# Optimization experiments

Hardware: AMD Instinct MI355X
Metric: run time of the kernel (lower is better)

Reference implementation:

```python
import jax, jax.numpy as jnp
import numpy as np

B, T, C, H = 4, 2048, 1024, 16
HD = C // H  # head_size = 64
EPS = 1e-5


def setup_inputs() -> dict:
    key = jax.random.key(0)
    ks = jax.random.split(key, 16)
    s_c = 1.0 / np.sqrt(C)
    s_4c = 1.0 / np.sqrt(4 * C)
    return {
        "x": jax.random.normal(ks[0], (B, T, C), jnp.float32),
        # per-head projections, stored [H, C, HD] (already in x@W orientation)
        "wq": jax.random.uniform(ks[1], (H, C, HD), jnp.float32, -s_c, s_c),
        "wk": jax.random.uniform(ks[2], (H, C, HD), jnp.float32, -s_c, s_c),
        "wv": jax.random.uniform(ks[3], (H, C, HD), jnp.float32, -s_c, s_c),
        "w_proj": jax.random.uniform(ks[4], (C, C), jnp.float32, -s_c, s_c),
        "b_proj": jax.random.uniform(ks[5], (C,), jnp.float32, -s_c, s_c),
        "w1": jax.random.uniform(ks[6], (C, 4 * C), jnp.float32, -s_c, s_c),
        "b1": jax.random.uniform(ks[7], (4 * C,), jnp.float32, -s_c, s_c),
        "w2": jax.random.uniform(ks[8], (4 * C, C), jnp.float32, -s_4c, s_4c),
        "b2": jax.random.uniform(ks[9], (C,), jnp.float32, -s_4c, s_4c),
        "ln1_g": jnp.ones((C,), jnp.float32),
        "ln1_b": jnp.zeros((C,), jnp.float32),
        "ln2_g": jnp.ones((C,), jnp.float32),
        "ln2_b": jnp.zeros((C,), jnp.float32),
    }


def layer_norm(x, g, b):
    mu = jnp.mean(x, axis=-1, keepdims=True)
    var = jnp.mean(jnp.square(x - mu), axis=-1, keepdims=True)
    return (x - mu) * jax.lax.rsqrt(var + EPS) * g + b


def reference(x, wq, wk, wv, w_proj, b_proj, w1, b1, w2, b2, ln1_g, ln1_b, ln2_g, ln2_b):
    Bc, Tc, Cc = x.shape
    h = layer_norm(x, ln1_g, ln1_b)
    q = jnp.einsum("btc,hcd->bhtd", h, wq)
    k = jnp.einsum("btc,hcd->bhtd", h, wk)
    v = jnp.einsum("btc,hcd->bhtd", h, wv)
    scale = HD ** -0.5
    wei = jnp.einsum("bhtd,bhsd->bhts", q, k) * scale  # [B,H,T,T]
    causal = jnp.tril(jnp.ones((Tc, Tc), bool))
    wei = jnp.where(causal, wei, -jnp.inf)
    wei = jax.nn.softmax(wei, axis=-1)
    att = jnp.einsum("bhts,bhsd->bhtd", wei, v)
    att = att.transpose(0, 2, 1, 3).reshape(Bc, Tc, Cc)  # concat heads
    x = x + att @ w_proj + b_proj
    h2 = layer_norm(x, ln2_g, ln2_b)
    ff = jax.nn.relu(h2 @ w1 + b1) @ w2 + b2
    return x + ff
```

## Files before the change

### kernel.cpp

```cpp
#include <hip/hip_runtime.h>


#define B_ 4
#define T_ 2048
#define C_ 1024
#define H_ 16
#define BT_ 8192

typedef __attribute__((ext_vector_type(8))) __bf16 bf16x8;
typedef __attribute__((ext_vector_type(4))) __bf16 bf16x4;
typedef __attribute__((ext_vector_type(4))) float f32x4;

#define WAIT_LGKM0 asm volatile("s_waitcnt lgkmcnt(0)" ::: "memory")
#define WAIT_VM4 asm volatile("s_waitcnt vmcnt(4)" ::: "memory")
#define WAIT_VM0 asm volatile("s_waitcnt vmcnt(0)" ::: "memory")

__device__ __forceinline__ void gload_lds16(const void* g, void* l) {
  __builtin_amdgcn_global_load_lds((const __attribute__((address_space(1))) void*)g,
                                   (__attribute__((address_space(3))) void*)l, 16, 0, 0);
}

__device__ __forceinline__ void block_sync() {
  asm volatile("" ::: "memory");
  __builtin_amdgcn_s_barrier();
  asm volatile("" ::: "memory");
}

__global__ __launch_bounds__(256) void transpose_f32_bf16(
    const float* __restrict__ in, __bf16* __restrict__ out,
    int R, int Cc, long inBatch, long outBatch) {
  __shared__ float tile[32][33];
  const int tx = threadIdx.x, ty = threadIdx.y;
  in += (long)blockIdx.z * inBatch;
  out += (long)blockIdx.z * outBatch;
  const int r0 = blockIdx.y * 32, c0 = blockIdx.x * 32;
#pragma unroll
  for (int i = 0; i < 4; i++)
    tile[ty + i * 8][tx] = in[(long)(r0 + ty + i * 8) * Cc + c0 + tx];
  __syncthreads();
#pragma unroll
  for (int i = 0; i < 4; i++)
    out[(long)(c0 + ty + i * 8) * R + r0 + tx] = (__bf16)tile[tx][ty + i * 8];
}

__global__ __launch_bounds__(256) void ln_fwd(const float* __restrict__ x,
                                              const float* __restrict__ g,
                                              const float* __restrict__ bta,
                                              __bf16* __restrict__ out) {
  const long row = blockIdx.x;
  const int tid = threadIdx.x;
  float4 v = ((const float4*)(x + row * C_))[tid];
  float vals[4] = {v.x, v.y, v.z, v.w};
  float s = vals[0] + vals[1] + vals[2] + vals[3];
  float s2 = vals[0] * vals[0] + vals[1] * vals[1] + vals[2] * vals[2] + vals[3] * vals[3];
#pragma unroll
  for (int o = 1; o < 64; o <<= 1) {
    s += __shfl_xor(s, o);
    s2 += __shfl_xor(s2, o);
  }
  __shared__ float red[8];
  const int lane = tid & 63, wid = tid >> 6;
  if (lane == 0) { red[wid] = s; red[wid + 4] = s2; }
  __syncthreads();
  const float S = red[0] + red[1] + red[2] + red[3];
  const float S2 = red[4] + red[5] + red[6] + red[7];
  const float mu = S * (1.0f / C_);
  const float var = S2 * (1.0f / C_) - mu * mu;
  const float rs = rsqrtf(var + 1e-5f);
  bf16x4 o4;
#pragma unroll
  for (int j = 0; j < 4; j++) {
    const int c = tid * 4 + j;
    o4[j] = (__bf16)((vals[j] - mu) * rs * g[c] + bta[c]);
  }
  *(bf16x4*)(out + row * C_ + tid * 4) = o4;
}

template <int OUT_BF16, int RELU, int HAS_BIAS, int HAS_RES, int TRANSO>
__global__ __launch_bounds__(256, 2) void gemm_bt(
    const __bf16* __restrict__ A, const __bf16* __restrict__ Bt, void* outp,
    const float* __restrict__ bias, const float* resid, int M, int N, int K) {
  __shared__ __bf16 As[128 * 32];
  __shared__ __bf16 Bs[128 * 32];
  const int tid = threadIdx.x, lane = tid & 63, wid = tid >> 6;
  const long mBase = (long)blockIdx.y * 128, nBase = (long)blockIdx.x * 128;
  const int wm = wid >> 1, wn = wid & 1;
  const int l15 = lane & 15, kHalf = (lane >> 4) * 8;
  f32x4 acc[4][4] = {};
  const int sRow = wid * 16 + (lane >> 2);
  const int sCol = (lane & 3) * 8;
  const __bf16* aP = A + (mBase + sRow) * (long)K + sCol;
  const __bf16* bP = Bt + (nBase + sRow) * (long)K + sCol;
  const int ldsOff = sRow * 32 + sCol;
  for (int kt = 0; kt < K; kt += 32) {
    gload_lds16(aP, As + ldsOff);
    gload_lds16(aP + 64 * (long)K, As + ldsOff + 2048);
    gload_lds16(bP, Bs + ldsOff);
    gload_lds16(bP + 64 * (long)K, Bs + ldsOff + 2048);
    aP += 32; bP += 32;
    __syncthreads();
    bf16x8 af[4], bfr[4];
#pragma unroll
    for (int mi = 0; mi < 4; mi++)
      af[mi] = *(const bf16x8*)&As[(wm * 64 + mi * 16 + l15) * 32 + kHalf];
#pragma unroll
    for (int ni = 0; ni < 4; ni++)
      bfr[ni] = *(const bf16x8*)&Bs[(wn * 64 + ni * 16 + l15) * 32 + kHalf];
#pragma unroll
    for (int mi = 0; mi < 4; mi++)
#pragma unroll
      for (int ni = 0; ni < 4; ni++)
        acc[mi][ni] = __builtin_amdgcn_mfma_f32_16x16x32_bf16(af[mi], bfr[ni], acc[mi][ni], 0, 0, 0);
    __syncthreads();
  }
#pragma unroll
  for (int mi = 0; mi < 4; mi++) {
#pragma unroll
    for (int ni = 0; ni < 4; ni++) {
      const long row0 = mBase + wm * 64 + mi * 16 + (lane >> 4) * 4;
      const long col = nBase + wn * 64 + ni * 16 + l15;
#pragma unroll
      for (int r = 0; r < 4; r++) {
        float vv = acc[mi][ni][r];
        if (HAS_BIAS) vv += bias[col];
        if (HAS_RES) vv += resid[(row0 + r) * N + col];
        if (RELU) vv = fmaxf(vv, 0.0f);
        if (OUT_BF16) {
          if (TRANSO) ((__bf16*)outp)[col * (long)M + row0 + r] = (__bf16)vv;
          else ((__bf16*)outp)[(row0 + r) * N + col] = (__bf16)vv;
        } else {
          ((float*)outp)[(row0 + r) * N + col] = vv;
        }
      }
    }
  }
}

template <int EPI>
__global__ __launch_bounds__(512, 2) void gemm256(
    const __bf16* __restrict__ A, const __bf16* __restrict__ Bt,
    void* out0, void* out1, void* out2,
    const float* __restrict__ bias, int M, int N, int K) {
  __shared__ __bf16 sm[3 * 16384];
  const int tid = threadIdx.x, lane = tid & 63, wid = tid >> 6;
  const int wm = wid >> 2, wn = wid & 3;
  const int l15 = lane & 15, qtr = lane >> 4;
  const long mBase = (long)blockIdx.y * 256, nBase = (long)blockIdx.x * 256;
  const int NT = K >> 5;

  f32x4 acc[8][4] = {};

  const int posOff = (qtr ^ ((l15 >> 1) & 3)) * 8;
  const int aBase = (wm * 128 + l15) * 32 + posOff;
  const int bBase = (wn * 64 + l15) * 32 + posOff;

  const int trow = tid >> 2;
  const long coff = (long)(((tid & 3) ^ ((tid >> 3) & 3)) * 8);
  const __bf16* aS0 = A + (mBase + trow) * (long)K + coff;
  const __bf16* aS1 = aS0 + 128 * (long)K;
  const __bf16* bS0 = Bt + (nBase + trow) * (long)K + coff;
  const __bf16* bS1 = bS0 + 128 * (long)K;

  {
    __bf16* d0 = &sm[0];
    gload_lds16(aS0, d0 + tid * 8);
    gload_lds16(aS1, d0 + 4096 + tid * 8);
    gload_lds16(bS0, d0 + 8192 + tid * 8);
    gload_lds16(bS1, d0 + 12288 + tid * 8);
    __bf16* d1 = &sm[16384];
    gload_lds16(aS0 + 32, d1 + tid * 8);
    gload_lds16(aS1 + 32, d1 + 4096 + tid * 8);
    gload_lds16(bS0 + 32, d1 + 8192 + tid * 8);
    gload_lds16(bS1 + 32, d1 + 12288 + tid * 8);
  }
  WAIT_VM4;
  block_sync();

  int sl = 0;
  for (int t = 0; t < NT; ++t) {
    const __bf16* sA = &sm[sl * 16384];
    const __bf16* sB = sA + 8192;
    const int slN = (sl + 2 >= 3) ? sl - 1 : sl + 2;
    __bf16* stA = &sm[slN * 16384];
    __bf16* stB = stA + 8192;
    const long kc = (long)(t + 2) * 32;
    const bool doStage = (t + 2 < NT);

    bf16x8 bfr[4], af[4];
#pragma unroll
    for (int cf = 0; cf < 4; cf++) bfr[cf] = *(const bf16x8*)&sB[bBase + cf * 512];
#pragma unroll
    for (int rf = 0; rf < 4; rf++) af[rf] = *(const bf16x8*)&sA[aBase + rf * 512];
    if (doStage) {
      gload_lds16(aS0 + kc, stA + tid * 8);
      gload_lds16(aS1 + kc, stA + 4096 + tid * 8);
    }
    block_sync();
    WAIT_LGKM0;
    __builtin_amdgcn_s_setprio(1);
#pragma unroll
    for (int rf = 0; rf < 4; rf++)
#pragma unroll
      for (int cf = 0; cf < 4; cf++)
        acc[rf][cf] = __builtin_amdgcn_mfma_f32_16x16x32_bf16(af[rf], bfr[cf], acc[rf][cf], 0, 0, 0);
    __builtin_amdgcn_s_setprio(0);
    block_sync();

#pragma unroll
    for (int rf = 0; rf < 4; rf++) af[rf] = *(const bf16x8*)&sA[aBase + 2048 + rf * 512];
    if (doStage) {
      gload_lds16(bS0 + kc, stB + tid * 8);
      gload_lds16(bS1 + kc, stB + 4096 + tid * 8);
      WAIT_VM4;
    } else {
      WAIT_VM0;
    }
    block_sync();
    WAIT_LGKM0;
    __builtin_amdgcn_s_setprio(1);
#pragma unroll
    for (int rf = 0; rf < 4; rf++)
#pragma unroll
      for (int cf = 0; cf < 4; cf++)
        acc[4 + rf][cf] = __builtin_amdgcn_mfma_f32_16x16x32_bf16(af[rf], bfr[cf], acc[4 + rf][cf], 0, 0, 0);
    __builtin_amdgcn_s_setprio(0);
    block_sync();

    sl = (sl + 1 == 3) ? 0 : sl + 1;
  }

  if (EPI == 0) {
    __bf16* outB = (__bf16*)out0;
#pragma unroll
    for (int cf = 0; cf < 4; cf++) {
      const long gc = nBase + wn * 64 + cf * 16 + l15;
      const float bv = bias[gc];
#pragma unroll
      for (int rfi = 0; rfi < 8; rfi++) {
        const long gr0 = mBase + wm * 128 + rfi * 16 + qtr * 4;
#pragma unroll
        for (int r = 0; r < 4; r++)
          outB[(gr0 + r) * (long)N + gc] = (__bf16)fmaxf(acc[rfi][cf][r] + bv, 0.0f);
      }
    }
  } else {
    const int seg = (int)(nBase >> 10);
#pragma unroll
    for (int cf = 0; cf < 4; cf++) {
      const long gc = nBase + wn * 64 + cf * 16 + l15;
      const long cc = gc & 1023;
#pragma unroll
      for (int rfi = 0; rfi < 8; rfi++) {
        const long gr0 = mBase + wm * 128 + rfi * 16 + qtr * 4;
        if (seg == 0) {
          __bf16* Qb = (__bf16*)out0;
#pragma unroll
          for (int r = 0; r < 4; r++) Qb[(gr0 + r) * 1024 + cc] = (__bf16)acc[rfi][cf][r];
        } else if (seg == 1) {
          __bf16* Kb = (__bf16*)out1;
#pragma unroll
          for (int r = 0; r < 4; r++) Kb[(gr0 + r) * 1024 + cc] = (__bf16)acc[rfi][cf][r];
        } else {
          __bf16* Vtg = (__bf16*)out2;
          bf16x4 v4;
#pragma unroll
          for (int r = 0; r < 4; r++) v4[r] = (__bf16)acc[rfi][cf][r];
          *(bf16x4*)&Vtg[cc * (long)BT_ + gr0] = v4;
        }
      }
    }
  }
}

#define PSTR 72
__global__ __launch_bounds__(512, 6) void attn_fwd2(
    const __bf16* __restrict__ Qg, const __bf16* __restrict__ Kg,
    const __bf16* __restrict__ Vtg, __bf16* __restrict__ O) {
  __shared__ __bf16 Ks[2][64 * 64];
  __shared__ __bf16 Vs[2][64 * 64];
  __shared__ __bf16 Ps[128 * PSTR];
  const int tid = threadIdx.x, lane = tid & 63, wid = tid >> 6;
  const int bh = blockIdx.y, b = bh >> 4, h = bh & 15;
  const int qx = 15 - blockIdx.x;
  const int qBase = qx * 128;
  const int qw = qBase + wid * 16;
  const int qwTop = qw + 15;
  const long bT = (long)b * T_;
  const int l15 = lane & 15, qtr = lane >> 4;
  const int q_lane = qw + l15;

  const int srow = tid >> 3;
  const int schunk = (tid & 7) ^ (srow & 7);
  const __bf16* kSrcBase = Kg + (bT + srow) * C_ + h * 64 + schunk * 8;
  const __bf16* vSrcBase = Vtg + (long)(h * 64 + srow) * BT_ + bT + schunk * 8;
  __bf16* kDst = &Ks[0][tid * 8];
  __bf16* vDst = &Vs[0][tid * 8];
  const int bufStride = 64 * 64;

  bf16x8 q0s, q1s;
  {
    bf16x8 r0 = *(const bf16x8*)(Qg + (bT + q_lane) * C_ + h * 64 + qtr * 8);
    bf16x8 r1 = *(const bf16x8*)(Qg + (bT + q_lane) * C_ + h * 64 + 32 + qtr * 8);
#pragma unroll
    for (int j = 0; j < 8; j++) {
      q0s[j] = (__bf16)((float)r0[j] * 0.125f);
      q1s[j] = (__bf16)((float)r1[j] * 0.125f);
    }
  }

  f32x4 o[4] = {};
  float m_ = -1e30f, l_ = 0.0f;
  const int nkt = 2 * qx + 2;

  gload_lds16(kSrcBase, kDst);
  gload_lds16(vSrcBase, vDst);
  __syncthreads();

  int buf = 0;
  for (int t = 0; t < nkt; t++) {
    const int k0 = t * 64;
    if (t + 1 < nkt) {
      const long koff = (long)(k0 + 64);
      gload_lds16(kSrcBase + koff * C_, kDst + (buf ^ 1) * bufStride);
      gload_lds16(vSrcBase + koff, vDst + (buf ^ 1) * bufStride);
    }
    if (k0 <= qwTop) {
      const __bf16* ks = Ks[buf];
      const __bf16* vs = Vs[buf];
      f32x4 sT[4] = {};
      __builtin_amdgcn_s_setprio(1);
#pragma unroll
      for (int kb = 0; kb < 4; kb++) {
        bf16x8 aK0 = *(const bf16x8*)&ks[(kb * 16 + l15) * 64 + ((qtr ^ (l15 & 7)) * 8)];
        bf16x8 aK1 = *(const bf16x8*)&ks[(kb * 16 + l15) * 64 + (((4 + qtr) ^ (l15 & 7)) * 8)];
        sT[kb] = __builtin_amdgcn_mfma_f32_16x16x32_bf16(aK0, q0s, sT[kb], 0, 0, 0);
        sT[kb] = __builtin_amdgcn_mfma_f32_16x16x32_bf16(aK1, q1s, sT[kb], 0, 0, 0);
      }
      __builtin_amdgcn_s_setprio(0);
      if (k0 + 63 > qw) {
#pragma unroll
        for (int kb = 0; kb < 4; kb++)
#pragma unroll
          for (int r = 0; r < 4; r++)
            if (k0 + kb * 16 + qtr * 4 + r > q_lane) sT[kb][r] = -1e30f;
      }
      float mx = -1e30f;
#pragma unroll
      for (int kb = 0; kb < 4; kb++)
#pragma unroll
        for (int r = 0; r < 4; r++) mx = fmaxf(mx, sT[kb][r]);
      mx = fmaxf(mx, __shfl_xor(mx, 16));
      mx = fmaxf(mx, __shfl_xor(mx, 32));
      const float mnew = fmaxf(m_, mx);
      const float fac = __expf(m_ - mnew);
      float psum = 0.0f;
#pragma unroll
      for (int kb = 0; kb < 4; kb++)
#pragma unroll
        for (int r = 0; r < 4; r++) {
          const float pv = __expf(sT[kb][r] - mnew);
          psum += pv;
          Ps[(wid * 16 + l15) * PSTR + kb * 16 + qtr * 4 + r] = (__bf16)pv;
        }
      psum += __shfl_xor(psum, 16);
      psum += __shfl_xor(psum, 32);
      l_ = l_ * fac + psum;
      m_ = mnew;
#pragma unroll
      for (int r = 0; r < 4; r++) {
        const float fr = __shfl(fac, (lane & 48) + qtr * 4 + r);
#pragma unroll
        for (int dg = 0; dg < 4; dg++) o[dg][r] *= fr;
      }
      __builtin_amdgcn_s_setprio(1);
#pragma unroll
      for (int s = 0; s < 2; s++) {
        bf16x8 aP = *(const bf16x8*)&Ps[(wid * 16 + l15) * PSTR + s * 32 + qtr * 8];
#pragma unroll
        for (int dg = 0; dg < 4; dg++) {
          bf16x8 bV = *(const bf16x8*)&vs[(dg * 16 + l15) * 64 + (((s * 4 + qtr) ^ (l15 & 7)) * 8)];
          o[dg] = __builtin_amdgcn_mfma_f32_16x16x32_bf16(aP, bV, o[dg], 0, 0, 0);
        }
      }
      __builtin_amdgcn_s_setprio(0);
    }
    __syncthreads();
    buf ^= 1;
  }

  const float linv = 1.0f / l_;
#pragma unroll
  for (int r = 0; r < 4; r++) {
    const float lr = __shfl(linv, (lane & 48) + qtr * 4 + r);
    const long row = bT + qw + qtr * 4 + r;
#pragma unroll
    for (int dg = 0; dg < 4; dg++)
      O[row * C_ + h * 64 + dg * 16 + l15] = (__bf16)(o[dg][r] * lr);
  }
}

extern "C" void kernel_launch(void* const* d_in, const int* in_sizes, int n_in,
                              void* d_out, int out_size, void* d_ws, size_t ws_size,
                              hipStream_t stream) {
  const float* x = (const float*)d_in[0];
  const float* wq = (const float*)d_in[1];
  const float* wk = (const float*)d_in[2];
  const float* wv = (const float*)d_in[3];
  const float* wproj = (const float*)d_in[4];
  const float* bproj = (const float*)d_in[5];
  const float* w1 = (const float*)d_in[6];
  const float* b1 = (const float*)d_in[7];
  const float* w2 = (const float*)d_in[8];
  const float* b2 = (const float*)d_in[9];
  const float* g1 = (const float*)d_in[10];
  const float* be1 = (const float*)d_in[11];
  const float* g2 = (const float*)d_in[12];
  const float* be2 = (const float*)d_in[13];

  char* ws = (char*)d_ws;
  const size_t MB = 1024ull * 1024ull;
  __bf16* h1 = (__bf16*)(ws + 0);
  __bf16* Qb = (__bf16*)(ws + 16 * MB);
  __bf16* Kb = (__bf16*)(ws + 32 * MB);
  __bf16* Vtg = (__bf16*)(ws + 48 * MB);
  __bf16* ff1 = (__bf16*)(ws + 32 * MB);
  __bf16* wqt = (__bf16*)(ws + 96 * MB);
  __bf16* wkt = (__bf16*)(ws + 98 * MB);
  __bf16* wvt = (__bf16*)(ws + 100 * MB);
  __bf16* wpt = (__bf16*)(ws + 102 * MB);
  __bf16* w1t = (__bf16*)(ws + 104 * MB);
  __bf16* w2t = (__bf16*)(ws + 112 * MB);
  __bf16* att = h1;
  __bf16* h2 = Qb;
  float* xout = (float*)d_out;

  dim3 tb(32, 8);
  transpose_f32_bf16<<<dim3(2, 32, 16), tb, 0, stream>>>(wq, wqt, 1024, 64, 1024 * 64, 64 * 1024);
  transpose_f32_bf16<<<dim3(2, 32, 16), tb, 0, stream>>>(wk, wkt, 1024, 64, 1024 * 64, 64 * 1024);
  transpose_f32_bf16<<<dim3(2, 32, 16), tb, 0, stream>>>(wv, wvt, 1024, 64, 1024 * 64, 64 * 1024);
  transpose_f32_bf16<<<dim3(32, 32, 1), tb, 0, stream>>>(wproj, wpt, 1024, 1024, 0, 0);
  transpose_f32_bf16<<<dim3(128, 32, 1), tb, 0, stream>>>(w1, w1t, 1024, 4096, 0, 0);
  transpose_f32_bf16<<<dim3(32, 128, 1), tb, 0, stream>>>(w2, w2t, 4096, 1024, 0, 0);

  ln_fwd<<<8192, 256, 0, stream>>>(x, g1, be1, h1);
  gemm256<1><<<dim3(12, 32), 512, 0, stream>>>(h1, wqt, Qb, Kb, Vtg, nullptr, 8192, 3072, 1024);
  attn_fwd2<<<dim3(16, 64), 512, 0, stream>>>(Qb, Kb, Vtg, att);
  gemm_bt<0, 0, 1, 1, 0><<<dim3(8, 64), 256, 0, stream>>>(att, wpt, xout, bproj, x, 8192, 1024, 1024);
  ln_fwd<<<8192, 256, 0, stream>>>(xout, g2, be2, h2);
  gemm256<0><<<dim3(16, 32), 512, 0, stream>>>(h2, w1t, ff1, nullptr, nullptr, b1, 8192, 4096, 1024);
  gemm_bt<0, 0, 1, 1, 0><<<dim3(8, 64), 256, 0, stream>>>(ff1, w2t, xout, b2, (const float*)xout, 8192, 1024, 4096);
}
```

Measured before the change: 467.4 us.

## Template GEMM on tile height; use it for proj/FFN2; lazy softmax rescale

Generalizes the triple-buffered 256-wide GEMM to a BM template and uses a 128x256 variant with a fused bias+residual fp32 epilogue for the projection and FFN2 GEMMs, replacing the simpler 128x128 gemm_bt. The QKV GEMM moves to the 128-row tile for more blocks. Attention now folds log2(e) into the Q scale and uses exp2f. It skips the running-max rescale when the new max exceeds the old by at most 8, and swaps the grid axes so blocks of the same head are ordered differently. These changes aim to raise MFMA efficiency and cut exp and rescale work, at the cost of larger fp32 exponent ranges under deferred maxima.

```diff
diff --git a/kernel.cpp b/kernel.cpp
--- a/kernel.cpp
+++ b/kernel.cpp
@@ -12,8 +12,7 @@
 typedef __attribute__((ext_vector_type(4))) float f32x4;
 
 #define WAIT_LGKM0 asm volatile("s_waitcnt lgkmcnt(0)" ::: "memory")
-#define WAIT_VM4 asm volatile("s_waitcnt vmcnt(4)" ::: "memory")
-#define WAIT_VM0 asm volatile("s_waitcnt vmcnt(0)" ::: "memory")
+#define WAIT_VM(N) asm volatile("s_waitcnt vmcnt(" #N ")" ::: "memory")
 
 __device__ __forceinline__ void gload_lds16(const void* g, void* l) {
   __builtin_amdgcn_global_load_lds((const __attribute__((address_space(1))) void*)g,
@@ -76,82 +75,27 @@
   *(bf16x4*)(out + row * C_ + tid * 4) = o4;
 }
 
-template <int OUT_BF16, int RELU, int HAS_BIAS, int HAS_RES, int TRANSO>
-__global__ __launch_bounds__(256, 2) void gemm_bt(
-    const __bf16* __restrict__ A, const __bf16* __restrict__ Bt, void* outp,
-    const float* __restrict__ bias, const float* resid, int M, int N, int K) {
-  __shared__ __bf16 As[128 * 32];
-  __shared__ __bf16 Bs[128 * 32];
-  const int tid = threadIdx.x, lane = tid & 63, wid = tid >> 6;
-  const long mBase = (long)blockIdx.y * 128, nBase = (long)blockIdx.x * 128;
-  const int wm = wid >> 1, wn = wid & 1;
-  const int l15 = lane & 15, kHalf = (lane >> 4) * 8;
-  f32x4 acc[4][4] = {};
-  const int sRow = wid * 16 + (lane >> 2);
-  const int sCol = (lane & 3) * 8;
-  const __bf16* aP = A + (mBase + sRow) * (long)K + sCol;
-  const __bf16* bP = Bt + (nBase + sRow) * (long)K + sCol;
-  const int ldsOff = sRow * 32 + sCol;
-  for (int kt = 0; kt < K; kt += 32) {
-    gload_lds16(aP, As + ldsOff);
-    gload_lds16(aP + 64 * (long)K, As + ldsOff + 2048);
-    gload_lds16(bP, Bs + ldsOff);
-    gload_lds16(bP + 64 * (long)K, Bs + ldsOff + 2048);
-    aP += 32; bP += 32;
-    __syncthreads();
-    bf16x8 af[4], bfr[4];
-#pragma unroll
-    for (int mi = 0; mi < 4; mi++)
-      af[mi] = *(const bf16x8*)&As[(wm * 64 + mi * 16 + l15) * 32 + kHalf];
-#pragma unroll
-    for (int ni = 0; ni < 4; ni++)
-      bfr[ni] = *(const bf16x8*)&Bs[(wn * 64 + ni * 16 + l15) * 32 + kHalf];
-#pragma unroll
-    for (int mi = 0; mi < 4; mi++)
-#pragma unroll
-      for (int ni = 0; ni < 4; ni++)
-        acc[mi][ni] = __builtin_amdgcn_mfma_f32_16x16x32_bf16(af[mi], bfr[ni], acc[mi][ni], 0, 0, 0);
-    __syncthreads();
-  }
-#pragma unroll
-  for (int mi = 0; mi < 4; mi++) {
-#pragma unroll
-    for (int ni = 0; ni < 4; ni++) {
-      const long row0 = mBase + wm * 64 + mi * 16 + (lane >> 4) * 4;
-      const long col = nBase + wn * 64 + ni * 16 + l15;
-#pragma unroll
-      for (int r = 0; r < 4; r++) {
-        float vv = acc[mi][ni][r];
-        if (HAS_BIAS) vv += bias[col];
-        if (HAS_RES) vv += resid[(row0 + r) * N + col];
-        if (RELU) vv = fmaxf(vv, 0.0f);
-        if (OUT_BF16) {
-          if (TRANSO) ((__bf16*)outp)[col * (long)M + row0 + r] = (__bf16)vv;
-          else ((__bf16*)outp)[(row0 + r) * N + col] = (__bf16)vv;
-        } else {
-          ((float*)outp)[(row0 + r) * N + col] = vv;
-        }
-      }
-    }
-  }
-}
-
-template <int EPI>
-__global__ __launch_bounds__(512, 2) void gemm256(
+template <int BM, int EPI>
+__global__ __launch_bounds__(512, 2) void gemm_mt(
     const __bf16* __restrict__ A, const __bf16* __restrict__ Bt,
     void* out0, void* out1, void* out2,
-    const float* __restrict__ bias, int M, int N, int K) {
-  __shared__ __bf16 sm[3 * 16384];
+    const float* __restrict__ bias, const float* __restrict__ resid,
+    int M, int N, int K) {
+  constexpr int SLOT = (BM + 256) * 32;
+  constexpr int ASZ = BM * 32;
+  constexpr int RF = BM / 32;
+  constexpr int WROW = BM / 2;
+  __shared__ __bf16 sm[3 * SLOT];
   const int tid = threadIdx.x, lane = tid & 63, wid = tid >> 6;
   const int wm = wid >> 2, wn = wid & 3;
   const int l15 = lane & 15, qtr = lane >> 4;
-  const long mBase = (long)blockIdx.y * 256, nBase = (long)blockIdx.x * 256;
+  const long mBase = (long)blockIdx.y * BM, nBase = (long)blockIdx.x * 256;
   const int NT = K >> 5;
 
-  f32x4 acc[8][4] = {};
+  f32x4 acc[RF][4] = {};
 
   const int posOff = (qtr ^ ((l15 >> 1) & 3)) * 8;
-  const int aBase = (wm * 128 + l15) * 32 + posOff;
+  const int aBase = (wm * WROW + l15) * 32 + posOff;
   const int bBase = (wn * 64 + l15) * 32 + posOff;
 
   const int trow = tid >> 2;
@@ -161,28 +105,25 @@
   const __bf16* bS0 = Bt + (nBase + trow) * (long)K + coff;
   const __bf16* bS1 = bS0 + 128 * (long)K;
 
-  {
-    __bf16* d0 = &sm[0];
-    gload_lds16(aS0, d0 + tid * 8);
-    gload_lds16(aS1, d0 + 4096 + tid * 8);
-    gload_lds16(bS0, d0 + 8192 + tid * 8);
-    gload_lds16(bS1, d0 + 12288 + tid * 8);
-    __bf16* d1 = &sm[16384];
-    gload_lds16(aS0 + 32, d1 + tid * 8);
-    gload_lds16(aS1 + 32, d1 + 4096 + tid * 8);
-    gload_lds16(bS0 + 32, d1 + 8192 + tid * 8);
-    gload_lds16(bS1 + 32, d1 + 12288 + tid * 8);
-  }
-  WAIT_VM4;
+#pragma unroll
+  for (int p = 0; p < 2; p++) {
+    __bf16* d = &sm[p * SLOT];
+    const long kc = (long)p * 32;
+    gload_lds16(aS0 + kc, d + tid * 8);
+    if (BM == 256) gload_lds16(aS1 + kc, d + 4096 + tid * 8);
+    gload_lds16(bS0 + kc, d + ASZ + tid * 8);
+    gload_lds16(bS1 + kc, d + ASZ + 4096 + tid * 8);
+  }
+  if (BM == 256) WAIT_VM(4); else WAIT_VM(3);
   block_sync();
 
   int sl = 0;
   for (int t = 0; t < NT; ++t) {
-    const __bf16* sA = &sm[sl * 16384];
-    const __bf16* sB = sA + 8192;
+    const __bf16* sA = &sm[sl * SLOT];
+    const __bf16* sB = sA + ASZ;
     const int slN = (sl + 2 >= 3) ? sl - 1 : sl + 2;
-    __bf16* stA = &sm[slN * 16384];
-    __bf16* stB = stA + 8192;
+    __bf16* stA = &sm[slN * SLOT];
+    __bf16* stB = stA + ASZ;
     const long kc = (long)(t + 2) * 32;
     const bool doStage = (t + 2 < NT);
 
@@ -191,41 +132,62 @@
     for (int cf = 0; cf < 4; cf++) bfr[cf] = *(const bf16x8*)&sB[bBase + cf * 512];
 #pragma unroll
     for (int rf = 0; rf < 4; rf++) af[rf] = *(const bf16x8*)&sA[aBase + rf * 512];
-    if (doStage) {
-      gload_lds16(aS0 + kc, stA + tid * 8);
-      gload_lds16(aS1 + kc, stA + 4096 + tid * 8);
-    }
-    block_sync();
-    WAIT_LGKM0;
-    __builtin_amdgcn_s_setprio(1);
-#pragma unroll
-    for (int rf = 0; rf < 4; rf++)
-#pragma unroll
-      for (int cf = 0; cf < 4; cf++)
-        acc[rf][cf] = __builtin_amdgcn_mfma_f32_16x16x32_bf16(af[rf], bfr[cf], acc[rf][cf], 0, 0, 0);
-    __builtin_amdgcn_s_setprio(0);
-    block_sync();
-
-#pragma unroll
-    for (int rf = 0; rf < 4; rf++) af[rf] = *(const bf16x8*)&sA[aBase + 2048 + rf * 512];
-    if (doStage) {
-      gload_lds16(bS0 + kc, stB + tid * 8);
-      gload_lds16(bS1 + kc, stB + 4096 + tid * 8);
-      WAIT_VM4;
+
+    if (BM == 256) {
+      if (doStage) {
+        gload_lds16(aS0 + kc, stA + tid * 8);
+        gload_lds16(aS1 + kc, stA + 4096 + tid * 8);
+      }
+      block_sync();
+      WAIT_LGKM0;
+      __builtin_amdgcn_s_setprio(1);
+#pragma unroll
+      for (int rf = 0; rf < 4; rf++)
+#pragma unroll
+        for (int cf = 0; cf < 4; cf++)
+          acc[rf][cf] = __builtin_amdgcn_mfma_f32_16x16x32_bf16(af[rf], bfr[cf], acc[rf][cf], 0, 0, 0);
+      __builtin_amdgcn_s_setprio(0);
+      block_sync();
+#pragma unroll
+      for (int rf = 0; rf < 4; rf++) af[rf] = *(const bf16x8*)&sA[aBase + 2048 + rf * 512];
+      if (doStage) {
+        gload_lds16(bS0 + kc, stB + tid * 8);
+        gload_lds16(bS1 + kc, stB + 4096 + tid * 8);
+        WAIT_VM(4);
+      } else {
+        WAIT_VM(0);
+      }
+      block_sync();
+      WAIT_LGKM0;
+      __builtin_amdgcn_s_setprio(1);
+#pragma unroll
+      for (int rf = 0; rf < 4; rf++)
+#pragma unroll
+        for (int cf = 0; cf < 4; cf++)
+          acc[(RF == 8 ? 4 : 0) + rf][cf] =
+              __builtin_amdgcn_mfma_f32_16x16x32_bf16(af[rf], bfr[cf], acc[(RF == 8 ? 4 : 0) + rf][cf], 0, 0, 0);
+      __builtin_amdgcn_s_setprio(0);
+      block_sync();
     } else {
-      WAIT_VM0;
-    }
-    block_sync();
-    WAIT_LGKM0;
-    __builtin_amdgcn_s_setprio(1);
-#pragma unroll
-    for (int rf = 0; rf < 4; rf++)
-#pragma unroll
-      for (int cf = 0; cf < 4; cf++)
-        acc[4 + rf][cf] = __builtin_amdgcn_mfma_f32_16x16x32_bf16(af[rf], bfr[cf], acc[4 + rf][cf], 0, 0, 0);
-    __builtin_amdgcn_s_setprio(0);
-    block_sync();
-
+      if (doStage) {
+        gload_lds16(aS0 + kc, stA + tid * 8);
+        gload_lds16(bS0 + kc, stB + tid * 8);
+        gload_lds16(bS1 + kc, stB + 4096 + tid * 8);
+        WAIT_VM(3);
+      } else {
+        WAIT_VM(0);
+      }
+      block_sync();
+      WAIT_LGKM0;
+      __builtin_amdgcn_s_setprio(1);
+#pragma unroll
+      for (int rf = 0; rf < 4; rf++)
+#pragma unroll
+        for (int cf = 0; cf < 4; cf++)
+          acc[rf][cf] = __builtin_amdgcn_mfma_f32_16x16x32_bf16(af[rf], bfr[cf], acc[rf][cf], 0, 0, 0);
+      __builtin_amdgcn_s_setprio(0);
+      block_sync();
+    }
     sl = (sl + 1 == 3) ? 0 : sl + 1;
   }
 
@@ -236,11 +198,25 @@
       const long gc = nBase + wn * 64 + cf * 16 + l15;
       const float bv = bias[gc];
 #pragma unroll
-      for (int rfi = 0; rfi < 8; rfi++) {
-        const long gr0 = mBase + wm * 128 + rfi * 16 + qtr * 4;
+      for (int rfi = 0; rfi < RF; rfi++) {
+        const long gr0 = mBase + wm * WROW + rfi * 16 + qtr * 4;
 #pragma unroll
         for (int r = 0; r < 4; r++)
           outB[(gr0 + r) * (long)N + gc] = (__bf16)fmaxf(acc[rfi][cf][r] + bv, 0.0f);
+      }
+    }
+  } else if (EPI == 2) {
+    float* outF = (float*)out0;
+#pragma unroll
+    for (int cf = 0; cf < 4; cf++) {
+      const long gc = nBase + wn * 64 + cf * 16 + l15;
+      const float bv = bias[gc];
+#pragma unroll
+      for (int rfi = 0; rfi < RF; rfi++) {
+        const long gr0 = mBase + wm * WROW + rfi * 16 + qtr * 4;
+#pragma unroll
+        for (int r = 0; r < 4; r++)
+          outF[(gr0 + r) * (long)N + gc] = acc[rfi][cf][r] + bv + resid[(gr0 + r) * (long)N + gc];
       }
     }
   } else {
@@ -250,8 +226,8 @@
       const long gc = nBase + wn * 64 + cf * 16 + l15;
       const long cc = gc & 1023;
 #pragma unroll
-      for (int rfi = 0; rfi < 8; rfi++) {
-        const long gr0 = mBase + wm * 128 + rfi * 16 + qtr * 4;
+      for (int rfi = 0; rfi < RF; rfi++) {
+        const long gr0 = mBase + wm * WROW + rfi * 16 + qtr * 4;
         if (seg == 0) {
           __bf16* Qb = (__bf16*)out0;
 #pragma unroll
@@ -280,8 +256,8 @@
   __shared__ __bf16 Vs[2][64 * 64];
   __shared__ __bf16 Ps[128 * PSTR];
   const int tid = threadIdx.x, lane = tid & 63, wid = tid >> 6;
-  const int bh = blockIdx.y, b = bh >> 4, h = bh & 15;
-  const int qx = 15 - blockIdx.x;
+  const int bh = blockIdx.x, b = bh >> 4, h = bh & 15;
+  const int qx = 15 - blockIdx.y;
   const int qBase = qx * 128;
   const int qw = qBase + wid * 16;
   const int qwTop = qw + 15;
@@ -299,12 +275,13 @@
 
   bf16x8 q0s, q1s;
   {
+    const float SC = 0.125f * 1.44269504089f;
     bf16x8 r0 = *(const bf16x8*)(Qg + (bT + q_lane) * C_ + h * 64 + qtr * 8);
     bf16x8 r1 = *(const bf16x8*)(Qg + (bT + q_lane) * C_ + h * 64 + 32 + qtr * 8);
 #pragma unroll
     for (int j = 0; j < 8; j++) {
-      q0s[j] = (__bf16)((float)r0[j] * 0.125f);
-      q1s[j] = (__bf16)((float)r1[j] * 0.125f);
+      q0s[j] = (__bf16)((float)r0[j] * SC);
+      q1s[j] = (__bf16)((float)r1[j] * SC);
     }
   }
 
@@ -351,26 +328,31 @@
         for (int r = 0; r < 4; r++) mx = fmaxf(mx, sT[kb][r]);
       mx = fmaxf(mx, __shfl_xor(mx, 16));
       mx = fmaxf(mx, __shfl_xor(mx, 32));
-      const float mnew = fmaxf(m_, mx);
-      const float fac = __expf(m_ - mnew);
+      const bool defer = __all(mx - m_ <= 8.0f);
+      const float mnew = defer ? m_ : fmaxf(m_, mx);
       float psum = 0.0f;
 #pragma unroll
       for (int kb = 0; kb < 4; kb++)
 #pragma unroll
         for (int r = 0; r < 4; r++) {
-          const float pv = __expf(sT[kb][r] - mnew);
+          const float pv = exp2f(sT[kb][r] - mnew);
           psum += pv;
           Ps[(wid * 16 + l15) * PSTR + kb * 16 + qtr * 4 + r] = (__bf16)pv;
         }
       psum += __shfl_xor(psum, 16);
       psum += __shfl_xor(psum, 32);
-      l_ = l_ * fac + psum;
-      m_ = mnew;
-#pragma unroll
-      for (int r = 0; r < 4; r++) {
-        const float fr = __shfl(fac, (lane & 48) + qtr * 4 + r);
-#pragma unroll
-        for (int dg = 0; dg < 4; dg++) o[dg][r] *= fr;
+      if (defer) {
+        l_ += psum;
+      } else {
+        const float fac = exp2f(m_ - mnew);
+        l_ = l_ * fac + psum;
+        m_ = mnew;
+#pragma unroll
+        for (int r = 0; r < 4; r++) {
+          const float fr = __shfl(fac, (lane & 48) + qtr * 4 + r);
+#pragma unroll
+          for (int dg = 0; dg < 4; dg++) o[dg][r] *= fr;
+        }
       }
       __builtin_amdgcn_s_setprio(1);
 #pragma unroll
@@ -443,10 +425,10 @@
   transpose_f32_bf16<<<dim3(32, 128, 1), tb, 0, stream>>>(w2, w2t, 4096, 1024, 0, 0);
 
   ln_fwd<<<8192, 256, 0, stream>>>(x, g1, be1, h1);
-  gemm256<1><<<dim3(12, 32), 512, 0, stream>>>(h1, wqt, Qb, Kb, Vtg, nullptr, 8192, 3072, 1024);
-  attn_fwd2<<<dim3(16, 64), 512, 0, stream>>>(Qb, Kb, Vtg, att);
-  gemm_bt<0, 0, 1, 1, 0><<<dim3(8, 64), 256, 0, stream>>>(att, wpt, xout, bproj, x, 8192, 1024, 1024);
+  gemm_mt<128, 1><<<dim3(12, 64), 512, 0, stream>>>(h1, wqt, Qb, Kb, Vtg, nullptr, nullptr, 8192, 3072, 1024);
+  attn_fwd2<<<dim3(64, 16), 512, 0, stream>>>(Qb, Kb, Vtg, att);
+  gemm_mt<128, 2><<<dim3(4, 64), 512, 0, stream>>>(att, wpt, xout, nullptr, nullptr, bproj, x, 8192, 1024, 1024);
   ln_fwd<<<8192, 256, 0, stream>>>(xout, g2, be2, h2);
-  gemm256<0><<<dim3(16, 32), 512, 0, stream>>>(h2, w1t, ff1, nullptr, nullptr, b1, 8192, 4096, 1024);
-  gemm_bt<0, 0, 1, 1, 0><<<dim3(8, 64), 256, 0, stream>>>(ff1, w2t, xout, b2, (const float*)xout, 8192, 1024, 4096);
-}
+  gemm_mt<256, 0><<<dim3(16, 32), 512, 0, stream>>>(h2, w1t, ff1, nullptr, nullptr, b1, nullptr, 8192, 4096, 1024);
+  gemm_mt<128, 2><<<dim3(4, 64), 512, 0, stream>>>(ff1, w2t, xout, nullptr, nullptr, b2, (const float*)xout, 8192, 1024, 4096);
+}
```

New measurement: 392.9 us. 15.9% less time.
